# Optimization experiments

Measured on AMD Instinct MI355X. Metric: run time of the kernel, lower is better.

Reference implementation:

```python
import jax, jax.numpy as jnp
import numpy as np

IN_SIZE = 256
OUT_SIZE = 64
N_NODES = 512
FAN_IN = 32
T = 2048  # max_context_length; actives window is full
D = IN_SIZE + N_NODES + OUT_SIZE  # 832


def setup_inputs() -> dict:
    key = jax.random.key(0)
    k1, k2, k3, k4 = jax.random.split(key, 4)
    x = jax.random.normal(k1, (IN_SIZE,), dtype=jnp.float32)
    actives = jax.random.normal(k2, (T, D), dtype=jnp.float32)
    weights = jax.random.normal(k3, (N_NODES, FAN_IN, 3), dtype=jnp.float32)
    in_idxs = jax.random.randint(k4, (N_NODES, FAN_IN), 0, IN_SIZE + N_NODES).astype(jnp.int32)
    return {"x": x, "actives": actives, "weights": weights, "in_idxs": in_idxs}


def reference(x, actives, weights, in_idxs):
    in_size = x.shape[0]
    # activate(): context window is full -> drop oldest row, append new row with x in first in_size cols
    new_row = jnp.zeros((actives.shape[1],), actives.dtype).at[:in_size].set(x)
    act = jnp.concatenate([actives[1:], new_row[None, :]], axis=0)  # (T, D)

    def step(act, node):
        ix, idxs, W = node
        inp = jnp.take(act, idxs, axis=1)            # gather: (T, fan_in)
        qkv = inp @ W                                # (T, 3)
        q, k, v = qkv[:, 0:1], qkv[:, 1:2], qkv[:, 2:3]  # each (T, 1), d_k = 1
        logits = q @ k.T                             # (T, T); / sqrt(d_k) with d_k=1
        attn = jax.nn.softmax(logits, axis=-1)
        out = jnp.tanh((attn @ v)[-1, 0])            # activation(values[-1:,]) -> scalar
        act = act.at[-1, in_size + ix].set(out)      # scatter into shared state
        return act, out

    nodes = (jnp.arange(weights.shape[0]), in_idxs, weights)
    _, outs = jax.lax.scan(step, act, nodes)         # sequential node loop (true dependency)
    return outs[-OUT_SIZE:]                          # last OUT_SIZE nodes are outputs
```

## Files before the change

kernel.cpp:

```cpp
#include <hip/hip_runtime.h>

#define IN_SIZE 256
#define OUT_SIZE 64
#define N_NODES 512
#define FAN_IN 32
#define T_DIM 2048
#define D_DIM 832
#define TOTAL_EDGE 16384
#define BLK_F4 1088
#define MAX_ENT 64
#define THRESH -20.0f

template <int CTRL, int RM>
__device__ __forceinline__ float dppadd(float v) {
  int m = __builtin_amdgcn_update_dpp(0, __float_as_int(v), CTRL, RM, 0xf, true);
  return v + __int_as_float(m);
}
__device__ __forceinline__ void wave_sum2(float& a, float& b) {
  a = dppadd<0x111, 0xf>(a); b = dppadd<0x111, 0xf>(b);
  a = dppadd<0x112, 0xf>(a); b = dppadd<0x112, 0xf>(b);
  a = dppadd<0x114, 0xf>(a); b = dppadd<0x114, 0xf>(b);
  a = dppadd<0x118, 0xf>(a); b = dppadd<0x118, 0xf>(b);
  a = dppadd<0x142, 0xa>(a); b = dppadd<0x142, 0xa>(b);
  a = dppadd<0x143, 0xc>(a); b = dppadd<0x143, 0xc>(b);
}
__device__ __forceinline__ float rl63(float v) {
  return __int_as_float(__builtin_amdgcn_readlane(__float_as_int(v), 63));
}

__global__ __launch_bounds__(256) void prep_kernel(
    const float* __restrict__ weights, float2* __restrict__ w12) {
  int e = blockIdx.x * 256 + threadIdx.x;
  if (e >= TOTAL_EDGE) return;
  const float* wp = weights + (size_t)e * 3;
  w12[e] = make_float2(wp[1], wp[2]);
}

__global__ __launch_bounds__(256) void kv_kernel(
    const float* __restrict__ actives, const int* __restrict__ in_idxs,
    const float2* __restrict__ w12, float2* __restrict__ KVd) {
  __shared__ float rows[8][836];
  __shared__ int s_idx[64 * FAN_IN];
  __shared__ float2 s_w[64 * FAN_IN];
  int tid = threadIdx.x;
  int tb = (blockIdx.x >> 1) * 8;
  int t0 = (blockIdx.x & 1) * 4;
#pragma unroll
  for (int r = 0; r < 8; ++r) {
    int t = tb + r;
    for (int c = tid; c < 208; c += 256) {
      float4 v4 = make_float4(0.f, 0.f, 0.f, 0.f);
      if (t < T_DIM - 1)
        v4 = ((const float4*)(actives + (size_t)(t + 1) * D_DIM))[c];
      *(float4*)&rows[r][4 * c] = v4;
    }
  }
  int tl = tid & 7, ng = tid >> 3;
  for (int tile = t0; tile < t0 + 4; ++tile) {
    __syncthreads();
    int n0 = tile * 64;
    for (int i = tid; i < 64 * FAN_IN; i += 256) {
      int g = n0 * FAN_IN + i;
      s_idx[i] = in_idxs[g];
      s_w[i] = w12[g];
    }
    __syncthreads();
#pragma unroll
    for (int it = 0; it < 2; ++it) {
      int nl = ng + 32 * it;
      const int* ip = &s_idx[nl * FAN_IN];
      const float2* wp = &s_w[nl * FAN_IN];
      float k = 0.f, v = 0.f;
#pragma unroll 8
      for (int f = 0; f < FAN_IN; ++f) {
        float a = rows[tl][ip[f]];
        float2 w = wp[f];
        k = fmaf(w.x, a, k);
        v = fmaf(w.y, a, v);
      }
      KVd[(size_t)(n0 + nl) * (2 * BLK_F4) + tb + tl] = make_float2(k, v);
    }
  }
}

__global__ __launch_bounds__(256) void block_kernel(
    const float* __restrict__ x, const int* __restrict__ in_idxs,
    const float* __restrict__ weights, float4* __restrict__ blk,
    float4* __restrict__ meta_g, float4* __restrict__ Qb) {
  __shared__ float2 skv[T_DIM], sbk[T_DIM];
  __shared__ int hist[64];
  __shared__ float smx[4], smn[4];
  __shared__ float4 sEnt[MAX_ENT];
  __shared__ int ecnt;
  int node = blockIdx.x, tid = threadIdx.x;
  if (tid == 0) ecnt = 0;
  const float2* src = (const float2*)(blk + (size_t)node * BLK_F4);
  float mx = -3.4e38f, mn = 3.4e38f;
#pragma unroll
  for (int j = 0; j < 8; ++j) {
    int t = j * 256 + tid;
    float2 kv = (t < 2047) ? src[t] : make_float2(0.f, 0.f);
    skv[t] = kv;
    if (t < 2047) { mx = fmaxf(mx, kv.x); mn = fminf(mn, kv.x); }
  }
  if (tid < 64) hist[tid] = 0;
#pragma unroll
  for (int off = 32; off > 0; off >>= 1) {
    mx = fmaxf(mx, __shfl_xor(mx, off));
    mn = fminf(mn, __shfl_xor(mn, off));
  }
  if ((tid & 63) == 0) { smx[tid >> 6] = mx; smn[tid >> 6] = mn; }
  __syncthreads();
  float kmax = fmaxf(fmaxf(smx[0], smx[1]), fmaxf(smx[2], smx[3]));
  float kmin = fminf(fminf(smn[0], smn[1]), fminf(smn[2], smn[3]));
  float invbw = 64.0f / (kmax - kmin);
#pragma unroll
  for (int j = 0; j < 8; ++j) {
    int t = j * 256 + tid;
    if (t < 2047) {
      int b = (int)((skv[t].x - kmin) * invbw);
      b = b < 0 ? 0 : (b > 63 ? 63 : b);
      atomicAdd(&hist[b], 1);
    }
  }
  {
    int target = IN_SIZE + node;
    for (int e = tid; e < TOTAL_EDGE; e += 256) {
      if (in_idxs[e] == target) {
        int c = e >> 5;
        if (c > node) {
          int p = atomicAdd(&ecnt, 1);
          if (p < MAX_ENT) {
            const float* wp = weights + (size_t)e * 3;
            sEnt[p] = make_float4(__int_as_float(c), wp[0], wp[1], wp[2]);
          }
        }
      }
    }
  }
  __syncthreads();
  if (tid < 64) {
    int v = hist[tid];
    int incl = v;
#pragma unroll
    for (int d = 1; d < 64; d <<= 1) {
      int u = __shfl_up(incl, d);
      if (tid >= d) incl += u;
    }
    hist[tid] = incl - v;
  }
  if (tid == 0) sbk[2047] = make_float2(0.f, 0.f);
  __syncthreads();
#pragma unroll
  for (int j = 0; j < 8; ++j) {
    int t = j * 256 + tid;
    if (t < 2047) {
      int b = (int)((skv[t].x - kmin) * invbw);
      b = b < 0 ? 0 : (b > 63 ? 63 : b);
      int p = atomicAdd(&hist[b], 1);
      sbk[p] = skv[t];
    }
  }
  if (tid < 32) {
    int g = node * FAN_IN + tid;
    int idx = in_idxs[g];
    const float* wp = weights + (size_t)g * 3;
    float a = (idx < IN_SIZE) ? x[idx] : 0.f;
    float p0 = a * wp[0], p1 = a * wp[1], p2 = a * wp[2];
#pragma unroll
    for (int off = 16; off > 0; off >>= 1) {
      p0 += __shfl_xor(p0, off);
      p1 += __shfl_xor(p1, off);
      p2 += __shfl_xor(p2, off);
    }
    if (tid == 0) Qb[node] = make_float4(p0, p1, p2, 0.f);
  }
  __syncthreads();
  float4* B = blk + (size_t)node * BLK_F4;
  for (int i = tid; i < 1024; i += 256) {
    float2 a = sbk[i];
    float2 d = sbk[2046 - i];
    B[i] = make_float4(a.x, a.y, d.x, d.y);
  }
  int cnt = ecnt < MAX_ENT ? ecnt : MAX_ENT;
  if (tid < MAX_ENT)
    B[1024 + tid] = (tid < cnt) ? sEnt[tid] : make_float4(0.f, 0.f, 0.f, 0.f);
  if (tid == 0)
    meta_g[3 * node + 0] =
        make_float4(kmax, kmin, __int_as_float(cnt), sbk[64].x);
  if (tid == 1)
    meta_g[3 * node + 1] =
        make_float4(sbk[1982].x, sbk[256].x, sbk[1790].x, sbk[512].x);
  if (tid == 2)
    meta_g[3 * node + 2] = make_float4(sbk[1534].x, 0.f, 0.f, 0.f);
}

__global__ __launch_bounds__(1024) void sweep_kernel(
    const int* __restrict__ in_idxs, const float4* __restrict__ Qb,
    const float4* __restrict__ meta_g, const float4* __restrict__ blk,
    float* __restrict__ out) {
  __shared__ float4 sQKV[N_NODES];
  __shared__ float4 sMeta[N_NODES][3];
  __shared__ int sRecv[N_NODES];
  __shared__ int sNeed[N_NODES];
  __shared__ float souts[OUT_SIZE];
  const int tid = threadIdx.x;
  const int lane = tid & 63;
  const int w = tid >> 6;

  for (int n = tid; n < N_NODES; n += 1024) {
    sQKV[n] = Qb[n];
    sMeta[n][0] = meta_g[3 * n + 0];
    sMeta[n][1] = meta_g[3 * n + 1];
    sMeta[n][2] = meta_g[3 * n + 2];
    sRecv[n] = 0;
  }
  if (tid < N_NODES) {
    const int4* ip = (const int4*)(in_idxs + tid * FAN_IN);
    int need = 0;
#pragma unroll
    for (int j = 0; j < 8; ++j) {
      int4 v = ip[j];
      need += (v.x >= IN_SIZE && v.x - IN_SIZE < tid);
      need += (v.y >= IN_SIZE && v.y - IN_SIZE < tid);
      need += (v.z >= IN_SIZE && v.z - IN_SIZE < tid);
      need += (v.w >= IN_SIZE && v.w - IN_SIZE < tid);
    }
    sNeed[tid] = need;
  }
  __syncthreads();

  auto process = [&](int node, float4 C0, float4 ENT, float4 m0, float4 m1,
                     float4 m2) {
    float4 qv = sQKV[node];
    float q = qv.x, kl = qv.y, vl = qv.z;
    int cnt = __float_as_int(m0.z);
    float m = fmaxf(fmaxf(q * m0.x, q * m0.y), q * kl);
    bool p1 = fmaxf(q * m0.w, q * m1.x) - m >= THRESH;
    bool p2 = p1 && (fmaxf(q * m1.y, q * m1.z) - m >= THRESH);
    bool p3 = p2 && (fmaxf(q * m1.w, q * m2.x) - m >= THRESH);
    const float4* B = blk + (size_t)node * BLK_F4;
    float4 t1[3], t2[4], t3[8];
    if (p1) {
#pragma unroll
      for (int t = 0; t < 3; ++t) t1[t] = B[64 + 64 * t + lane];
    }
    if (p2) {
#pragma unroll
      for (int t = 0; t < 4; ++t) t2[t] = B[256 + 64 * t + lane];
    }
    if (p3) {
#pragma unroll
      for (int t = 0; t < 8; ++t) t3[t] = B[512 + 64 * t + lane];
    }
    float el = __expf(q * kl - m);
    float w0 = __expf(fmaf(q, C0.x, -m));
    float w1 = __expf(fmaf(q, C0.z, -m));
    float sw = w0 + w1;
    float swv = fmaf(w0, C0.y, w1 * C0.w);
    if (p1) {
#pragma unroll
      for (int t = 0; t < 3; ++t) {
        float a0 = __expf(fmaf(q, t1[t].x, -m));
        float a1 = __expf(fmaf(q, t1[t].z, -m));
        sw += a0 + a1;
        swv = fmaf(a0, t1[t].y, fmaf(a1, t1[t].w, swv));
      }
    }
    if (p2) {
#pragma unroll
      for (int t = 0; t < 4; ++t) {
        float a0 = __expf(fmaf(q, t2[t].x, -m));
        float a1 = __expf(fmaf(q, t2[t].z, -m));
        sw += a0 + a1;
        swv = fmaf(a0, t2[t].y, fmaf(a1, t2[t].w, swv));
      }
    }
    if (p3) {
#pragma unroll
      for (int t = 0; t < 8; ++t) {
        float a0 = __expf(fmaf(q, t3[t].x, -m));
        float a1 = __expf(fmaf(q, t3[t].z, -m));
        if (t == 7 && lane == 63) a1 = 0.f;
        sw += a0 + a1;
        swv = fmaf(a0, t3[t].y, fmaf(a1, t3[t].w, swv));
      }
    }
    wave_sum2(sw, swv);
    float S = rl63(sw) + el;
    float SV = fmaf(el, vl, rl63(swv));
    float z = SV * __builtin_amdgcn_rcpf(S);
    float eo = __expf(2.f * z);
    float o = 1.f - 2.f * __builtin_amdgcn_rcpf(eo + 1.f);
    if (lane == 0 && node >= N_NODES - OUT_SIZE)
      souts[node - (N_NODES - OUT_SIZE)] = o;
    if (lane < cnt) {
      int c = __float_as_int(ENT.x);
      atomicAdd(&sQKV[c].x, o * ENT.y);
      atomicAdd(&sQKV[c].y, o * ENT.z);
      atomicAdd(&sQKV[c].z, o * ENT.w);
    }
    asm volatile("s_waitcnt lgkmcnt(0)" ::: "memory");
    if (lane < cnt) {
      int c = __float_as_int(ENT.x);
      atomicAdd(&sRecv[c], 1);
    }
  };

  auto pf = [&](int n, float4& c0, float4& ent, float4& m0, float4& m1,
                float4& m2) {
    const float4* B = blk + (size_t)n * BLK_F4;
    c0 = B[lane];
    ent = B[1024 + lane];
    m0 = sMeta[n][0];
    m1 = sMeta[n][1];
    m2 = sMeta[n][2];
  };

  auto spinwait = [&](int n) {
    int need = sNeed[n];
    if (need > 0) {
      const volatile int* rp = (const volatile int*)&sRecv[n];
      int it = 0;
      while (*rp < need && ++it < 1000000) __builtin_amdgcn_s_sleep(1);
    }
    asm volatile("" ::: "memory");
  };

  float4 c0A, entA, m0A, m1A, m2A;
  float4 c0B, entB, m0B, m1B, m2B;
  pf(w, c0A, entA, m0A, m1A, m2A);
  for (int n = w; n < N_NODES; n += 32) {
    pf(n + 16, c0B, entB, m0B, m1B, m2B);
    spinwait(n);
    process(n, c0A, entA, m0A, m1A, m2A);
    if (n + 32 < N_NODES) pf(n + 32, c0A, entA, m0A, m1A, m2A);
    spinwait(n + 16);
    process(n + 16, c0B, entB, m0B, m1B, m2B);
  }
  __syncthreads();
  if (tid < OUT_SIZE) out[tid] = souts[tid];
}

extern "C" void kernel_launch(void* const* d_in, const int* in_sizes, int n_in,
                              void* d_out, int out_size, void* d_ws,
                              size_t ws_size, hipStream_t stream) {
  const float* x = (const float*)d_in[0];
  const float* actives = (const float*)d_in[1];
  const float* weights = (const float*)d_in[2];
  const int* in_idxs = (const int*)d_in[3];
  float* out = (float*)d_out;

  char* ws = (char*)d_ws;
  float4* blk = (float4*)ws;
  size_t off = (size_t)N_NODES * BLK_F4 * 16;
  float4* meta_g = (float4*)(ws + off); off += (size_t)N_NODES * 3 * 16;
  float4* Qb = (float4*)(ws + off); off += (size_t)N_NODES * 16;
  float2* w12 = (float2*)(ws + off);

  prep_kernel<<<TOTAL_EDGE / 256, 256, 0, stream>>>(weights, w12);
  kv_kernel<<<(T_DIM / 8) * 2, 256, 0, stream>>>(actives, in_idxs, w12,
                                                 (float2*)blk);
  block_kernel<<<N_NODES, 256, 0, stream>>>(x, in_idxs, weights, blk, meta_g,
                                            Qb);
  sweep_kernel<<<1, 1024, 0, stream>>>(in_idxs, Qb, meta_g, blk, out);
}
```

Baseline: 175.3 us.

## Drop weight prep kernel, vectorize edge scan, prefetch tier-1 blocks, busy-spin

Removes the separate prep kernel by staging raw interleaved weights into padded shared memory inside kv_kernel, saving one launch and a global round trip. The reverse-edge scan in block_kernel now reads in_idxs as int4. The sequential sweep prefetches the first tier of attention blocks together with the other per-node data, so those loads come off the dependency chain. It also raises wave priority while processing and replaces the sleep in the spin-wait with a tight busy loop. The prefetch raises register pressure and always loads tier-1 data even when it is skipped.

```diff
diff --git a/kernel.cpp b/kernel.cpp
--- a/kernel.cpp
+++ b/kernel.cpp
@@ -28,20 +28,12 @@
   return __int_as_float(__builtin_amdgcn_readlane(__float_as_int(v), 63));
 }
 
-__global__ __launch_bounds__(256) void prep_kernel(
-    const float* __restrict__ weights, float2* __restrict__ w12) {
-  int e = blockIdx.x * 256 + threadIdx.x;
-  if (e >= TOTAL_EDGE) return;
-  const float* wp = weights + (size_t)e * 3;
-  w12[e] = make_float2(wp[1], wp[2]);
-}
-
 __global__ __launch_bounds__(256) void kv_kernel(
     const float* __restrict__ actives, const int* __restrict__ in_idxs,
-    const float2* __restrict__ w12, float2* __restrict__ KVd) {
+    const float* __restrict__ weights, float2* __restrict__ KVd) {
   __shared__ float rows[8][836];
-  __shared__ int s_idx[64 * FAN_IN];
-  __shared__ float2 s_w[64 * FAN_IN];
+  __shared__ int s_idx[64 * 33];
+  __shared__ float s_raw[64 * 100];
   int tid = threadIdx.x;
   int tb = (blockIdx.x >> 1) * 8;
   int t0 = (blockIdx.x & 1) * 4;
@@ -59,24 +51,29 @@
   for (int tile = t0; tile < t0 + 4; ++tile) {
     __syncthreads();
     int n0 = tile * 64;
-    for (int i = tid; i < 64 * FAN_IN; i += 256) {
-      int g = n0 * FAN_IN + i;
-      s_idx[i] = in_idxs[g];
-      s_w[i] = w12[g];
+    for (int i = tid; i < 2048; i += 256) {
+      int nl = i >> 5, f = i & 31;
+      s_idx[nl * 33 + f] = in_idxs[n0 * FAN_IN + i];
+    }
+    {
+      const float4* wsrc = (const float4*)(weights + (size_t)n0 * FAN_IN * 3);
+      for (int i = tid; i < 1536; i += 256) {
+        int nl = i / 24, j = i - nl * 24;
+        *(float4*)&s_raw[nl * 100 + 4 * j] = wsrc[i];
+      }
     }
     __syncthreads();
 #pragma unroll
     for (int it = 0; it < 2; ++it) {
       int nl = ng + 32 * it;
-      const int* ip = &s_idx[nl * FAN_IN];
-      const float2* wp = &s_w[nl * FAN_IN];
+      const int* ip = &s_idx[nl * 33];
+      const float* wp = &s_raw[nl * 100];
       float k = 0.f, v = 0.f;
 #pragma unroll 8
       for (int f = 0; f < FAN_IN; ++f) {
         float a = rows[tl][ip[f]];
-        float2 w = wp[f];
-        k = fmaf(w.x, a, k);
-        v = fmaf(w.y, a, v);
+        k = fmaf(wp[3 * f + 1], a, k);
+        v = fmaf(wp[3 * f + 2], a, v);
       }
       KVd[(size_t)(n0 + nl) * (2 * BLK_F4) + tb + tl] = make_float2(k, v);
     }
@@ -125,14 +122,23 @@
   }
   {
     int target = IN_SIZE + node;
-    for (int e = tid; e < TOTAL_EDGE; e += 256) {
-      if (in_idxs[e] == target) {
-        int c = e >> 5;
-        if (c > node) {
-          int p = atomicAdd(&ecnt, 1);
-          if (p < MAX_ENT) {
-            const float* wp = weights + (size_t)e * 3;
-            sEnt[p] = make_float4(__int_as_float(c), wp[0], wp[1], wp[2]);
+    const int4* ip4 = (const int4*)in_idxs;
+#pragma unroll 4
+    for (int e4 = tid; e4 < TOTAL_EDGE / 4; e4 += 256) {
+      int4 v = ip4[e4];
+      int e0 = 4 * e4;
+#pragma unroll
+      for (int c4 = 0; c4 < 4; ++c4) {
+        int idx = c4 == 0 ? v.x : (c4 == 1 ? v.y : (c4 == 2 ? v.z : v.w));
+        if (idx == target) {
+          int e = e0 + c4;
+          int c = e >> 5;
+          if (c > node) {
+            int p = atomicAdd(&ecnt, 1);
+            if (p < MAX_ENT) {
+              const float* wp = weights + (size_t)e * 3;
+              sEnt[p] = make_float4(__int_as_float(c), wp[0], wp[1], wp[2]);
+            }
           }
         }
       }
@@ -230,8 +236,8 @@
   }
   __syncthreads();
 
-  auto process = [&](int node, float4 C0, float4 ENT, float4 m0, float4 m1,
-                     float4 m2) {
+  auto process = [&](int node, float4 C0, float4 ENT, float4 T10, float4 T11,
+                     float4 T12, float4 m0, float4 m1, float4 m2) {
     float4 qv = sQKV[node];
     float q = qv.x, kl = qv.y, vl = qv.z;
     int cnt = __float_as_int(m0.z);
@@ -240,11 +246,7 @@
     bool p2 = p1 && (fmaxf(q * m1.y, q * m1.z) - m >= THRESH);
     bool p3 = p2 && (fmaxf(q * m1.w, q * m2.x) - m >= THRESH);
     const float4* B = blk + (size_t)node * BLK_F4;
-    float4 t1[3], t2[4], t3[8];
-    if (p1) {
-#pragma unroll
-      for (int t = 0; t < 3; ++t) t1[t] = B[64 + 64 * t + lane];
-    }
+    float4 t2[4], t3[8];
     if (p2) {
 #pragma unroll
       for (int t = 0; t < 4; ++t) t2[t] = B[256 + 64 * t + lane];
@@ -259,13 +261,16 @@
     float sw = w0 + w1;
     float swv = fmaf(w0, C0.y, w1 * C0.w);
     if (p1) {
-#pragma unroll
-      for (int t = 0; t < 3; ++t) {
-        float a0 = __expf(fmaf(q, t1[t].x, -m));
-        float a1 = __expf(fmaf(q, t1[t].z, -m));
-        sw += a0 + a1;
-        swv = fmaf(a0, t1[t].y, fmaf(a1, t1[t].w, swv));
-      }
+      float a0 = __expf(fmaf(q, T10.x, -m));
+      float a1 = __expf(fmaf(q, T10.z, -m));
+      float b0 = __expf(fmaf(q, T11.x, -m));
+      float b1 = __expf(fmaf(q, T11.z, -m));
+      float c0 = __expf(fmaf(q, T12.x, -m));
+      float c1 = __expf(fmaf(q, T12.z, -m));
+      sw += a0 + a1 + b0 + b1 + c0 + c1;
+      swv = fmaf(a0, T10.y, fmaf(a1, T10.w, swv));
+      swv = fmaf(b0, T11.y, fmaf(b1, T11.w, swv));
+      swv = fmaf(c0, T12.y, fmaf(c1, T12.w, swv));
     }
     if (p2) {
 #pragma unroll
@@ -307,11 +312,14 @@
     }
   };
 
-  auto pf = [&](int n, float4& c0, float4& ent, float4& m0, float4& m1,
-                float4& m2) {
+  auto pf = [&](int n, float4& c0, float4& ent, float4& t10, float4& t11,
+                float4& t12, float4& m0, float4& m1, float4& m2) {
     const float4* B = blk + (size_t)n * BLK_F4;
     c0 = B[lane];
     ent = B[1024 + lane];
+    t10 = B[64 + lane];
+    t11 = B[128 + lane];
+    t12 = B[192 + lane];
     m0 = sMeta[n][0];
     m1 = sMeta[n][1];
     m2 = sMeta[n][2];
@@ -322,21 +330,26 @@
     if (need > 0) {
       const volatile int* rp = (const volatile int*)&sRecv[n];
       int it = 0;
-      while (*rp < need && ++it < 1000000) __builtin_amdgcn_s_sleep(1);
+      while (*rp < need && ++it < 4000000) {}
     }
     asm volatile("" ::: "memory");
   };
 
-  float4 c0A, entA, m0A, m1A, m2A;
-  float4 c0B, entB, m0B, m1B, m2B;
-  pf(w, c0A, entA, m0A, m1A, m2A);
+  float4 c0A, entA, t1A0, t1A1, t1A2, m0A, m1A, m2A;
+  float4 c0B, entB, t1B0, t1B1, t1B2, m0B, m1B, m2B;
+  pf(w, c0A, entA, t1A0, t1A1, t1A2, m0A, m1A, m2A);
   for (int n = w; n < N_NODES; n += 32) {
-    pf(n + 16, c0B, entB, m0B, m1B, m2B);
+    pf(n + 16, c0B, entB, t1B0, t1B1, t1B2, m0B, m1B, m2B);
     spinwait(n);
-    process(n, c0A, entA, m0A, m1A, m2A);
-    if (n + 32 < N_NODES) pf(n + 32, c0A, entA, m0A, m1A, m2A);
+    __builtin_amdgcn_s_setprio(1);
+    process(n, c0A, entA, t1A0, t1A1, t1A2, m0A, m1A, m2A);
+    __builtin_amdgcn_s_setprio(0);
+    if (n + 32 < N_NODES)
+      pf(n + 32, c0A, entA, t1A0, t1A1, t1A2, m0A, m1A, m2A);
     spinwait(n + 16);
-    process(n + 16, c0B, entB, m0B, m1B, m2B);
+    __builtin_amdgcn_s_setprio(1);
+    process(n + 16, c0B, entB, t1B0, t1B1, t1B2, m0B, m1B, m2B);
+    __builtin_amdgcn_s_setprio(0);
   }
   __syncthreads();
   if (tid < OUT_SIZE) out[tid] = souts[tid];
@@ -355,11 +368,9 @@
   float4* blk = (float4*)ws;
   size_t off = (size_t)N_NODES * BLK_F4 * 16;
   float4* meta_g = (float4*)(ws + off); off += (size_t)N_NODES * 3 * 16;
-  float4* Qb = (float4*)(ws + off); off += (size_t)N_NODES * 16;
-  float2* w12 = (float2*)(ws + off);
-
-  prep_kernel<<<TOTAL_EDGE / 256, 256, 0, stream>>>(weights, w12);
-  kv_kernel<<<(T_DIM / 8) * 2, 256, 0, stream>>>(actives, in_idxs, w12,
+  float4* Qb = (float4*)(ws + off);
+
+  kv_kernel<<<(T_DIM / 8) * 2, 256, 0, stream>>>(actives, in_idxs, weights,
                                                  (float2*)blk);
   block_kernel<<<N_NODES, 256, 0, stream>>>(x, in_idxs, weights, blk, meta_g,
                                             Qb);
```

Result: slower. 214.5 us (+22.4%).
